# Kernel tuning notes

Hardware: AMD Instinct MI355X
Metric: run time of the kernel (lower is better)

The kernel has to match this reference:

```python
import jax, jax.numpy as jnp
import numpy as np

N, D, NUM_CLASSES = 4096, 1024, 10


def setup_inputs() -> dict:
    key = jax.random.key(0)
    k1, k2, k3 = jax.random.split(key, 3)
    return {
        "fm_s": jax.random.normal(k1, (N, D), dtype=jnp.float32),
        "fm_t": jax.random.normal(k2, (N, D), dtype=jnp.float32),
        "targets": jax.random.randint(k3, (N,), 0, NUM_CLASSES, dtype=jnp.int64),
        "fusion_true": 0,
    }


def reference(fm_s, fm_t, targets, fusion_true):
    # fusion_true == False branch of CL.forward (multi_index unused).
    # Pairwise squared distances ||s_i - t_j||^2 via the GEMM expansion
    # instead of materializing the [N, N, D] difference tensor.
    s2 = jnp.sum(fm_s * fm_s, axis=-1)            # [N]
    t2 = jnp.sum(fm_t * fm_t, axis=-1)            # [N]
    cross = jnp.einsum('id,jd->ij', fm_s, fm_t)   # [N, N]
    d2 = s2[:, None] + t2[None, :] - 2.0 * cross  # [N, N]

    # self_mask_pos[i, j] = 1 where targets[i] == targets[j]
    mask_pos = (targets[:, None] == targets[None, :]).astype(d2.dtype)  # [N, N]
    row_norm = jnp.sum(mask_pos, axis=-1, keepdims=True)                # [N, 1], >= 1

    loss_pos = d2 * mask_pos / row_norm           # [N, N]
    return jnp.mean(jnp.sum(loss_pos, axis=-1))   # scalar
```

## Files before the change

### kernel.cpp

```cpp
#include <hip/hip_runtime.h>

#define N_ROWS 4096
#define D_DIM  1024
#define NCLS   10


#define CHUNK     32
#define NCHUNK    (N_ROWS / CHUNK)
#define SLICE_W   512
#define NSLICE    (D_DIM / SLICE_W)
#define K1_BLOCKS (2 * NSLICE * NCHUNK)
#define K2_BLOCKS 40
#define CS        (NCLS * SLICE_W)

#define OFF_CTR   0
#define OFF_ACC2  16
#define OFF_DOTP  (OFF_ACC2 + K1_BLOCKS)
#define OFF_PART  544
#define PART_FLOATS (NSLICE * NCHUNK * NCLS * SLICE_W)
#define NEED_FLOATS (OFF_PART + 2 * PART_FLOATS)

#define OFF_FBS   544
#define FB_FLOATS (OFF_FBS + 2 * NCLS * D_DIM)

__global__ __launch_bounds__(256) void k_pass1(const float* __restrict__ fm_s,
                                               const float* __restrict__ fm_t,
                                               const int* __restrict__ tgt,
                                               float* __restrict__ ws) {
    const int bid = blockIdx.x, tid = threadIdx.x;
    const int mat   = bid >> 8;
    const int rem   = bid & 255;
    const int slice = rem >> 7;
    const int chunk = rem & 127;

    if (bid == 0 && tid == 0) ((int*)ws)[OFF_CTR] = 0;

    __shared__ int tl[CHUNK];
    if (tid < CHUNK) tl[tid] = tgt[chunk * CHUNK + tid];
    __syncthreads();

    const float* src  = mat ? fm_t : fm_s;
    const float* base = src + (size_t)chunk * CHUNK * D_DIM + slice * SLICE_W + tid * 2;

    float2 a[NCLS];
#pragma unroll
    for (int k = 0; k < NCLS; ++k) a[k] = make_float2(0.f, 0.f);
    float acc2 = 0.f;

#pragma unroll
    for (int r0 = 0; r0 < CHUNK; r0 += 16) {
        float2 v[16];
#pragma unroll
        for (int j = 0; j < 16; ++j)
            v[j] = *(const float2*)(base + (size_t)(r0 + j) * D_DIM);
#pragma unroll
        for (int j = 0; j < 16; ++j) {
            const float x = v[j].x, y = v[j].y;
            acc2 += x * x + y * y;
            const int c = __builtin_amdgcn_readfirstlane(tl[r0 + j]);
            switch (c) {
                case 0: a[0].x += x; a[0].y += y; break;
                case 1: a[1].x += x; a[1].y += y; break;
                case 2: a[2].x += x; a[2].y += y; break;
                case 3: a[3].x += x; a[3].y += y; break;
                case 4: a[4].x += x; a[4].y += y; break;
                case 5: a[5].x += x; a[5].y += y; break;
                case 6: a[6].x += x; a[6].y += y; break;
                case 7: a[7].x += x; a[7].y += y; break;
                case 8: a[8].x += x; a[8].y += y; break;
                default: a[9].x += x; a[9].y += y; break;
            }
        }
    }

    float* part = ws + OFF_PART + (size_t)mat * PART_FLOATS
                + (size_t)(slice * NCHUNK + chunk) * CS + tid * 2;
#pragma unroll
    for (int k = 0; k < NCLS; ++k)
        *(float2*)(part + (size_t)k * SLICE_W) = a[k];

    __shared__ float red[256];
    red[tid] = acc2;
    __syncthreads();
    for (int s = 128; s > 0; s >>= 1) {
        if (tid < s) red[tid] += red[tid + s];
        __syncthreads();
    }
    if (tid == 0) ws[OFF_ACC2 + bid] = red[0];
}

__global__ __launch_bounds__(256) void k_pass2(const int* __restrict__ tgt,
                                               float* __restrict__ ws,
                                               float* __restrict__ out) {
    const int b = blockIdx.x, tid = threadIdx.x;
    const int cls  = b >> 2;
    const int colq = b & 3;
    const int g    = tid >> 6;
    const int ct   = tid & 63;
    const int mat  = g >> 1;
    const int half = g & 1;
    const int slice = colq >> 1;
    const int c512  = (colq & 1) * 256 + ct * 4;

    const float* p = ws + OFF_PART + (size_t)mat * PART_FLOATS
                   + (size_t)slice * ((size_t)NCHUNK * CS)
                   + (size_t)(half * 64) * CS
                   + (size_t)cls * SLICE_W + c512;

    float4 s0 = {0,0,0,0}, s1 = {0,0,0,0}, s2 = {0,0,0,0}, s3 = {0,0,0,0};
#pragma unroll
    for (int c0 = 0; c0 < 64; c0 += 16) {
        float4 v[16];
#pragma unroll
        for (int j = 0; j < 16; ++j)
            v[j] = *(const float4*)(p + (size_t)(c0 + j) * CS);
#pragma unroll
        for (int j = 0; j < 16; ++j) {
            float4& acc = ((j & 3) == 0) ? s0 : ((j & 3) == 1) ? s1 : ((j & 3) == 2) ? s2 : s3;
            acc.x += v[j].x; acc.y += v[j].y; acc.z += v[j].z; acc.w += v[j].w;
        }
    }
    float4 sum;
    sum.x = (s0.x + s1.x) + (s2.x + s3.x);
    sum.y = (s0.y + s1.y) + (s2.y + s3.y);
    sum.z = (s0.z + s1.z) + (s2.z + s3.z);
    sum.w = (s0.w + s1.w) + (s2.w + s3.w);

    __shared__ float4 red4[4][64];
    red4[g][ct] = sum;
    __syncthreads();

    __shared__ float prodRed[64];
    if (tid < 64) {
        float4 A, B;
        A.x = red4[0][tid].x + red4[1][tid].x;
        A.y = red4[0][tid].y + red4[1][tid].y;
        A.z = red4[0][tid].z + red4[1][tid].z;
        A.w = red4[0][tid].w + red4[1][tid].w;
        B.x = red4[2][tid].x + red4[3][tid].x;
        B.y = red4[2][tid].y + red4[3][tid].y;
        B.z = red4[2][tid].z + red4[3][tid].z;
        B.w = red4[2][tid].w + red4[3][tid].w;
        prodRed[tid] = A.x * B.x + A.y * B.y + A.z * B.z + A.w * B.w;
    }
    __syncthreads();
    for (int s = 32; s > 0; s >>= 1) {
        if (tid < s) prodRed[tid] += prodRed[tid + s];
        __syncthreads();
    }

    __shared__ int isLast;
    if (tid == 0) {
        ws[OFF_DOTP + b] = prodRed[0];
        __threadfence();
        int old = atomicAdd((int*)ws + OFF_CTR, 1);
        isLast = (old == K2_BLOCKS - 1) ? 1 : 0;
    }
    __syncthreads();
    if (!isLast) return;
    __threadfence();

    __shared__ int hist[NCLS];
    if (tid < NCLS) hist[tid] = 0;
    __syncthreads();
    for (int i = tid; i < N_ROWS; i += 256) atomicAdd(&hist[tgt[i]], 1);
    __syncthreads();

    double v = (double)ws[OFF_ACC2 + tid] + (double)ws[OFF_ACC2 + tid + 256];
    if (tid < K2_BLOCKS) {
        int n = hist[tid >> 2];
        if (n > 0) v -= 2.0 * (double)ws[OFF_DOTP + tid] / (double)n;
    }
    __shared__ double dred[256];
    dred[tid] = v;
    __syncthreads();
    for (int s = 128; s > 0; s >>= 1) {
        if (tid < s) dred[tid] += dred[tid + s];
        __syncthreads();
    }
    if (tid == 0) out[0] = (float)(dred[0] / (double)N_ROWS);
}

__global__ void k_fb_zero(float* __restrict__ ws) {
    int i = blockIdx.x * 256 + threadIdx.x;
    if (i < 2 * NCLS * D_DIM) ws[OFF_FBS + i] = 0.f;
}

__global__ __launch_bounds__(256) void k_fb_acc(const float* __restrict__ fm_s,
                                                const float* __restrict__ fm_t,
                                                const int* __restrict__ tgt,
                                                float* __restrict__ ws) {
    const int bid = blockIdx.x, tid = threadIdx.x;
    const int mat   = bid >> 8;
    const int rem   = bid & 255;
    const int slice = rem >> 7;
    const int chunk = rem & 127;

    __shared__ int tl[CHUNK];
    if (tid < CHUNK) tl[tid] = tgt[chunk * CHUNK + tid];
    __syncthreads();

    const float* src  = mat ? fm_t : fm_s;
    const float* base = src + (size_t)chunk * CHUNK * D_DIM + slice * SLICE_W + tid * 2;

    float2 a[NCLS];
#pragma unroll
    for (int k = 0; k < NCLS; ++k) a[k] = make_float2(0.f, 0.f);
    float acc2 = 0.f;

    for (int r = 0; r < CHUNK; ++r) {
        float2 v = *(const float2*)(base + (size_t)r * D_DIM);
        acc2 += v.x * v.x + v.y * v.y;
        const int c = __builtin_amdgcn_readfirstlane(tl[r]);
        switch (c) {
            case 0: a[0].x += v.x; a[0].y += v.y; break;
            case 1: a[1].x += v.x; a[1].y += v.y; break;
            case 2: a[2].x += v.x; a[2].y += v.y; break;
            case 3: a[3].x += v.x; a[3].y += v.y; break;
            case 4: a[4].x += v.x; a[4].y += v.y; break;
            case 5: a[5].x += v.x; a[5].y += v.y; break;
            case 6: a[6].x += v.x; a[6].y += v.y; break;
            case 7: a[7].x += v.x; a[7].y += v.y; break;
            case 8: a[8].x += v.x; a[8].y += v.y; break;
            default: a[9].x += v.x; a[9].y += v.y; break;
        }
    }

    int col = slice * SLICE_W + tid * 2;
    float* dst = ws + OFF_FBS + (size_t)mat * NCLS * D_DIM + col;
#pragma unroll
    for (int k = 0; k < NCLS; ++k) {
        atomicAdd(dst + (size_t)k * D_DIM,     a[k].x);
        atomicAdd(dst + (size_t)k * D_DIM + 1, a[k].y);
    }

    __shared__ float red[256];
    red[tid] = acc2;
    __syncthreads();
    for (int s = 128; s > 0; s >>= 1) {
        if (tid < s) red[tid] += red[tid + s];
        __syncthreads();
    }
    if (tid == 0) ws[OFF_ACC2 + bid] = red[0];
}

__global__ __launch_bounds__(256) void k_fb_fin(const int* __restrict__ tgt,
                                                float* __restrict__ ws,
                                                float* __restrict__ out) {
    const int tid = threadIdx.x;
    __shared__ int hist[NCLS];
    if (tid < NCLS) hist[tid] = 0;
    __syncthreads();
    for (int i = tid; i < N_ROWS; i += 256) atomicAdd(&hist[tgt[i]], 1);
    __syncthreads();

    double v = (double)ws[OFF_ACC2 + tid] + (double)ws[OFF_ACC2 + tid + 256];
    for (int i = tid; i < NCLS * D_DIM; i += 256) {
        int n = hist[i >> 10];
        if (n > 0) {
            double sS = ws[OFF_FBS + i];
            double sT = ws[OFF_FBS + NCLS * D_DIM + i];
            v -= 2.0 * sS * sT / (double)n;
        }
    }
    __shared__ double dred[256];
    dred[tid] = v;
    __syncthreads();
    for (int s = 128; s > 0; s >>= 1) {
        if (tid < s) dred[tid] += dred[tid + s];
        __syncthreads();
    }
    if (tid == 0) out[0] = (float)(dred[0] / (double)N_ROWS);
}

extern "C" void kernel_launch(void* const* d_in, const int* in_sizes, int n_in,
                              void* d_out, int out_size, void* d_ws, size_t ws_size,
                              hipStream_t stream) {
    const float* fm_s = (const float*)d_in[0];
    const float* fm_t = (const float*)d_in[1];
    const int*   tgt  = (const int*)d_in[2];

    float* ws   = (float*)d_ws;
    float* outp = (float*)d_out;

    if (ws_size >= (size_t)NEED_FLOATS * sizeof(float)) {
        k_pass1<<<K1_BLOCKS, 256, 0, stream>>>(fm_s, fm_t, tgt, ws);
        k_pass2<<<K2_BLOCKS, 256, 0, stream>>>(tgt, ws, outp);
    } else {
        k_fb_zero<<<(2 * NCLS * D_DIM + 255) / 256, 256, 0, stream>>>(ws);
        k_fb_acc<<<K1_BLOCKS, 256, 0, stream>>>(fm_s, fm_t, tgt, ws);
        k_fb_fin<<<1, 256, 0, stream>>>(tgt, ws, outp);
    }
}
```

Baseline: 29.73 us.

## Widen pass1 to full-row float4 loads and spread pass2 reduction over more blocks

Pass 1 now uses 256 blocks, each covering a full 1024-wide row chunk with float4 loads, instead of 512 blocks on half-width slices with float2. This halves the block count and doubles the work per thread. Pass 2 is reorganised into 160 blocks (class x 64-column tiles) with a shared-memory tree reduction, to spread the partial-sum reduction more widely. The class histogram in the last block is now built from per-thread register counts instead of shared atomics. Fewer pass-1 blocks on a large GPU may reduce memory-level parallelism, and each thread now holds 40 accumulator floats, which raises register pressure.

```diff
diff --git a/kernel.cpp b/kernel.cpp
--- a/kernel.cpp
+++ b/kernel.cpp
@@ -7,31 +7,27 @@
 
 #define CHUNK     32
 #define NCHUNK    (N_ROWS / CHUNK)
-#define SLICE_W   512
-#define NSLICE    (D_DIM / SLICE_W)
-#define K1_BLOCKS (2 * NSLICE * NCHUNK)
-#define K2_BLOCKS 40
-#define CS        (NCLS * SLICE_W)
+#define K1_BLOCKS 256
+#define K2_BLOCKS 160
+#define PART_FLOATS (NCHUNK * NCLS * D_DIM)
 
 #define OFF_CTR   0
 #define OFF_ACC2  16
-#define OFF_DOTP  (OFF_ACC2 + K1_BLOCKS)
-#define OFF_PART  544
-#define PART_FLOATS (NSLICE * NCHUNK * NCLS * SLICE_W)
+#define OFF_DOTP  528
+#define OFF_PART  688
 #define NEED_FLOATS (OFF_PART + 2 * PART_FLOATS)
 
-#define OFF_FBS   544
-#define FB_FLOATS (OFF_FBS + 2 * NCLS * D_DIM)
+#define FB_SLICE_W 512
+#define FB_OFF_SUM 688
+#define FB_NEED    (FB_OFF_SUM + 2 * NCLS * D_DIM)
 
 __global__ __launch_bounds__(256) void k_pass1(const float* __restrict__ fm_s,
                                                const float* __restrict__ fm_t,
                                                const int* __restrict__ tgt,
                                                float* __restrict__ ws) {
     const int bid = blockIdx.x, tid = threadIdx.x;
-    const int mat   = bid >> 8;
-    const int rem   = bid & 255;
-    const int slice = rem >> 7;
-    const int chunk = rem & 127;
+    const int mat   = bid >> 7;
+    const int chunk = bid & 127;
 
     if (bid == 0 && tid == 0) ((int*)ws)[OFF_CTR] = 0;
 
@@ -40,44 +36,44 @@
     __syncthreads();
 
     const float* src  = mat ? fm_t : fm_s;
-    const float* base = src + (size_t)chunk * CHUNK * D_DIM + slice * SLICE_W + tid * 2;
-
-    float2 a[NCLS];
-#pragma unroll
-    for (int k = 0; k < NCLS; ++k) a[k] = make_float2(0.f, 0.f);
+    const float* base = src + (size_t)chunk * CHUNK * D_DIM + tid * 4;
+
+    float4 a[NCLS];
+#pragma unroll
+    for (int k = 0; k < NCLS; ++k) a[k] = make_float4(0.f, 0.f, 0.f, 0.f);
     float acc2 = 0.f;
 
 #pragma unroll
     for (int r0 = 0; r0 < CHUNK; r0 += 16) {
-        float2 v[16];
+        float4 v[16];
 #pragma unroll
         for (int j = 0; j < 16; ++j)
-            v[j] = *(const float2*)(base + (size_t)(r0 + j) * D_DIM);
+            v[j] = *(const float4*)(base + (size_t)(r0 + j) * D_DIM);
 #pragma unroll
         for (int j = 0; j < 16; ++j) {
-            const float x = v[j].x, y = v[j].y;
-            acc2 += x * x + y * y;
+            const float4 w = v[j];
+            acc2 += w.x * w.x + w.y * w.y + w.z * w.z + w.w * w.w;
             const int c = __builtin_amdgcn_readfirstlane(tl[r0 + j]);
             switch (c) {
-                case 0: a[0].x += x; a[0].y += y; break;
-                case 1: a[1].x += x; a[1].y += y; break;
-                case 2: a[2].x += x; a[2].y += y; break;
-                case 3: a[3].x += x; a[3].y += y; break;
-                case 4: a[4].x += x; a[4].y += y; break;
-                case 5: a[5].x += x; a[5].y += y; break;
-                case 6: a[6].x += x; a[6].y += y; break;
-                case 7: a[7].x += x; a[7].y += y; break;
-                case 8: a[8].x += x; a[8].y += y; break;
-                default: a[9].x += x; a[9].y += y; break;
+                case 0: a[0].x += w.x; a[0].y += w.y; a[0].z += w.z; a[0].w += w.w; break;
+                case 1: a[1].x += w.x; a[1].y += w.y; a[1].z += w.z; a[1].w += w.w; break;
+                case 2: a[2].x += w.x; a[2].y += w.y; a[2].z += w.z; a[2].w += w.w; break;
+                case 3: a[3].x += w.x; a[3].y += w.y; a[3].z += w.z; a[3].w += w.w; break;
+                case 4: a[4].x += w.x; a[4].y += w.y; a[4].z += w.z; a[4].w += w.w; break;
+                case 5: a[5].x += w.x; a[5].y += w.y; a[5].z += w.z; a[5].w += w.w; break;
+                case 6: a[6].x += w.x; a[6].y += w.y; a[6].z += w.z; a[6].w += w.w; break;
+                case 7: a[7].x += w.x; a[7].y += w.y; a[7].z += w.z; a[7].w += w.w; break;
+                case 8: a[8].x += w.x; a[8].y += w.y; a[8].z += w.z; a[8].w += w.w; break;
+                default: a[9].x += w.x; a[9].y += w.y; a[9].z += w.z; a[9].w += w.w; break;
             }
         }
     }
 
     float* part = ws + OFF_PART + (size_t)mat * PART_FLOATS
-                + (size_t)(slice * NCHUNK + chunk) * CS + tid * 2;
+                + (size_t)chunk * (NCLS * D_DIM) + tid * 4;
 #pragma unroll
     for (int k = 0; k < NCLS; ++k)
-        *(float2*)(part + (size_t)k * SLICE_W) = a[k];
+        *(float4*)(part + (size_t)k * D_DIM) = a[k];
 
     __shared__ float red[256];
     red[tid] = acc2;
@@ -93,65 +89,55 @@
                                                float* __restrict__ ws,
                                                float* __restrict__ out) {
     const int b = blockIdx.x, tid = threadIdx.x;
-    const int cls  = b >> 2;
-    const int colq = b & 3;
-    const int g    = tid >> 6;
-    const int ct   = tid & 63;
-    const int mat  = g >> 1;
-    const int half = g & 1;
-    const int slice = colq >> 1;
-    const int c512  = (colq & 1) * 256 + ct * 4;
-
-    const float* p = ws + OFF_PART + (size_t)mat * PART_FLOATS
-                   + (size_t)slice * ((size_t)NCHUNK * CS)
-                   + (size_t)(half * 64) * CS
-                   + (size_t)cls * SLICE_W + c512;
-
-    float4 s0 = {0,0,0,0}, s1 = {0,0,0,0}, s2 = {0,0,0,0}, s3 = {0,0,0,0};
-#pragma unroll
-    for (int c0 = 0; c0 < 64; c0 += 16) {
-        float4 v[16];
-#pragma unroll
-        for (int j = 0; j < 16; ++j)
-            v[j] = *(const float4*)(p + (size_t)(c0 + j) * CS);
-#pragma unroll
-        for (int j = 0; j < 16; ++j) {
-            float4& acc = ((j & 3) == 0) ? s0 : ((j & 3) == 1) ? s1 : ((j & 3) == 2) ? s2 : s3;
-            acc.x += v[j].x; acc.y += v[j].y; acc.z += v[j].z; acc.w += v[j].w;
-        }
-    }
-    float4 sum;
-    sum.x = (s0.x + s1.x) + (s2.x + s3.x);
-    sum.y = (s0.y + s1.y) + (s2.y + s3.y);
-    sum.z = (s0.z + s1.z) + (s2.z + s3.z);
-    sum.w = (s0.w + s1.w) + (s2.w + s3.w);
-
-    __shared__ float4 red4[4][64];
-    red4[g][ct] = sum;
-    __syncthreads();
-
-    __shared__ float prodRed[64];
-    if (tid < 64) {
-        float4 A, B;
-        A.x = red4[0][tid].x + red4[1][tid].x;
-        A.y = red4[0][tid].y + red4[1][tid].y;
-        A.z = red4[0][tid].z + red4[1][tid].z;
-        A.w = red4[0][tid].w + red4[1][tid].w;
-        B.x = red4[2][tid].x + red4[3][tid].x;
-        B.y = red4[2][tid].y + red4[3][tid].y;
-        B.z = red4[2][tid].z + red4[3][tid].z;
-        B.w = red4[2][tid].w + red4[3][tid].w;
-        prodRed[tid] = A.x * B.x + A.y * B.y + A.z * B.z + A.w * B.w;
-    }
-    __syncthreads();
-    for (int s = 32; s > 0; s >>= 1) {
-        if (tid < s) prodRed[tid] += prodRed[tid + s];
-        __syncthreads();
-    }
+    const int cls  = b >> 4;
+    const int bcol = (b & 15) * 64;
+    const int grp  = tid >> 4;
+    const int pos  = tid & 15;
+
+    const size_t cstride = NCLS * D_DIM;
+    const float* baseS = ws + OFF_PART + (size_t)(grp * 8) * cstride
+                       + (size_t)cls * D_DIM + bcol + pos * 4;
+    const float* baseT = baseS + PART_FLOATS;
+
+    float4 aS = make_float4(0, 0, 0, 0), aT = make_float4(0, 0, 0, 0);
+#pragma unroll
+    for (int j = 0; j < 8; ++j) {
+        float4 vS = *(const float4*)(baseS + (size_t)j * cstride);
+        float4 vT = *(const float4*)(baseT + (size_t)j * cstride);
+        aS.x += vS.x; aS.y += vS.y; aS.z += vS.z; aS.w += vS.w;
+        aT.x += vT.x; aT.y += vT.y; aT.z += vT.z; aT.w += vT.w;
+    }
+
+    __shared__ float4 sS[16][16], sT[16][16];
+    sS[grp][pos] = aS;
+    sT[grp][pos] = aT;
+    __syncthreads();
+    for (int h = 8; h > 0; h >>= 1) {
+        if (grp < h) {
+            float4 x = sS[grp + h][pos], y = sS[grp][pos];
+            y.x += x.x; y.y += x.y; y.z += x.z; y.w += x.w;
+            sS[grp][pos] = y;
+            x = sT[grp + h][pos]; y = sT[grp][pos];
+            y.x += x.x; y.y += x.y; y.z += x.z; y.w += x.w;
+            sT[grp][pos] = y;
+        }
+        __syncthreads();
+    }
+
+    __shared__ float dred[16];
+    if (tid < 16) {
+        float4 S = sS[0][tid], T = sT[0][tid];
+        dred[tid] = S.x * T.x + S.y * T.y + S.z * T.z + S.w * T.w;
+    }
+    __syncthreads();
+    if (tid < 8) dred[tid] += dred[tid + 8];
+    __syncthreads();
+    if (tid < 4) dred[tid] += dred[tid + 4];
+    __syncthreads();
 
     __shared__ int isLast;
     if (tid == 0) {
-        ws[OFF_DOTP + b] = prodRed[0];
+        ws[OFF_DOTP + b] = (dred[0] + dred[1]) + (dred[2] + dred[3]);
         __threadfence();
         int old = atomicAdd((int*)ws + OFF_CTR, 1);
         isLast = (old == K2_BLOCKS - 1) ? 1 : 0;
@@ -160,30 +146,45 @@
     if (!isLast) return;
     __threadfence();
 
+    int cnt[NCLS];
+#pragma unroll
+    for (int k = 0; k < NCLS; ++k) cnt[k] = 0;
+#pragma unroll
+    for (int j = 0; j < 16; ++j) {
+        int c = tgt[tid * 16 + j];
+#pragma unroll
+        for (int k = 0; k < NCLS; ++k) cnt[k] += (c == k) ? 1 : 0;
+    }
+    __shared__ int hl[256 * NCLS];
+#pragma unroll
+    for (int k = 0; k < NCLS; ++k) hl[tid * NCLS + k] = cnt[k];
+    __syncthreads();
     __shared__ int hist[NCLS];
-    if (tid < NCLS) hist[tid] = 0;
-    __syncthreads();
-    for (int i = tid; i < N_ROWS; i += 256) atomicAdd(&hist[tgt[i]], 1);
-    __syncthreads();
-
-    double v = (double)ws[OFF_ACC2 + tid] + (double)ws[OFF_ACC2 + tid + 256];
+    if (tid < NCLS) {
+        int s = 0;
+        for (int i = 0; i < 256; ++i) s += hl[i * NCLS + tid];
+        hist[tid] = s;
+    }
+    __syncthreads();
+
+    double v = (double)ws[OFF_ACC2 + tid];
     if (tid < K2_BLOCKS) {
-        int n = hist[tid >> 2];
+        int n = hist[tid >> 4];
         if (n > 0) v -= 2.0 * (double)ws[OFF_DOTP + tid] / (double)n;
     }
-    __shared__ double dred[256];
-    dred[tid] = v;
-    __syncthreads();
-    for (int s = 128; s > 0; s >>= 1) {
-        if (tid < s) dred[tid] += dred[tid + s];
-        __syncthreads();
-    }
-    if (tid == 0) out[0] = (float)(dred[0] / (double)N_ROWS);
+    __shared__ double fr[256];
+    fr[tid] = v;
+    __syncthreads();
+    for (int s = 128; s > 0; s >>= 1) {
+        if (tid < s) fr[tid] += fr[tid + s];
+        __syncthreads();
+    }
+    if (tid == 0) out[0] = (float)(fr[0] / (double)N_ROWS);
 }
 
 __global__ void k_fb_zero(float* __restrict__ ws) {
     int i = blockIdx.x * 256 + threadIdx.x;
-    if (i < 2 * NCLS * D_DIM) ws[OFF_FBS + i] = 0.f;
+    if (i < 2 * NCLS * D_DIM) ws[FB_OFF_SUM + i] = 0.f;
 }
 
 __global__ __launch_bounds__(256) void k_fb_acc(const float* __restrict__ fm_s,
@@ -201,7 +202,7 @@
     __syncthreads();
 
     const float* src  = mat ? fm_t : fm_s;
-    const float* base = src + (size_t)chunk * CHUNK * D_DIM + slice * SLICE_W + tid * 2;
+    const float* base = src + (size_t)chunk * CHUNK * D_DIM + slice * FB_SLICE_W + tid * 2;
 
     float2 a[NCLS];
 #pragma unroll
@@ -226,8 +227,8 @@
         }
     }
 
-    int col = slice * SLICE_W + tid * 2;
-    float* dst = ws + OFF_FBS + (size_t)mat * NCLS * D_DIM + col;
+    int col = slice * FB_SLICE_W + tid * 2;
+    float* dst = ws + FB_OFF_SUM + (size_t)mat * NCLS * D_DIM + col;
 #pragma unroll
     for (int k = 0; k < NCLS; ++k) {
         atomicAdd(dst + (size_t)k * D_DIM,     a[k].x);
@@ -258,8 +259,8 @@
     for (int i = tid; i < NCLS * D_DIM; i += 256) {
         int n = hist[i >> 10];
         if (n > 0) {
-            double sS = ws[OFF_FBS + i];
-            double sT = ws[OFF_FBS + NCLS * D_DIM + i];
+            double sS = ws[FB_OFF_SUM + i];
+            double sT = ws[FB_OFF_SUM + NCLS * D_DIM + i];
             v -= 2.0 * sS * sT / (double)n;
         }
     }
@@ -288,7 +289,7 @@
         k_pass2<<<K2_BLOCKS, 256, 0, stream>>>(tgt, ws, outp);
     } else {
         k_fb_zero<<<(2 * NCLS * D_DIM + 255) / 256, 256, 0, stream>>>(ws);
-        k_fb_acc<<<K1_BLOCKS, 256, 0, stream>>>(fm_s, fm_t, tgt, ws);
+        k_fb_acc<<<512, 256, 0, stream>>>(fm_s, fm_t, tgt, ws);
         k_fb_fin<<<1, 256, 0, stream>>>(tgt, ws, outp);
     }
 }
```

Measured after the change: 33.32 us. 12.1% more time.
